# Optimization experiments

Measured on AMD Instinct MI355X. Metric: run time of the kernel, lower is better.

The kernel has to match this reference:

```python
import jax, jax.numpy as jnp
import numpy as np

B, S, H = 1, 2048, 1024
NH, HD = 16, 64          # num heads, head dim (H = NH*HD)
NT = 1024                # param token num (qkv_slot_num = proj_slot_num)


def pattention(x, key_tokens, value_tokens):
    """Pattention with gelu_l2_norm: x:[...,H] -> [...,out]."""
    attn = jnp.einsum('bsh,th->bst', x, key_tokens)          # scale_factor = 1
    g = jax.nn.gelu(attn, approximate=False)                 # torch F.gelu exact
    norm = jnp.linalg.norm(g, axis=-1, keepdims=True)
    w = g / norm * jnp.sqrt(jnp.asarray(g.shape[-1], g.dtype))
    return jnp.einsum('bst,td->bsd', w, value_tokens)


def setup_inputs() -> dict:
    key = jax.random.key(0)
    ks = jax.random.split(key, 9)
    names = ['q_key', 'q_val', 'k_key', 'k_val', 'v_key', 'v_val', 'proj_key', 'proj_val']
    inp = {'x': jax.random.normal(ks[0], (B, S, H), jnp.float32)}
    for i, n in enumerate(names):
        inp[n] = jax.random.normal(ks[i + 1], (NT, H), jnp.float32) * 0.02
    return inp


def reference(x, q_key, q_val, k_key, k_val, v_key, v_val, proj_key, proj_val):
    # Q/K/V via Pattention (token-parameter attention)
    q = pattention(x, q_key, q_val).reshape(B, S, NH, HD)
    k = pattention(x, k_key, k_val).reshape(B, S, NH, HD)
    v = pattention(x, v_key, v_val).reshape(B, S, NH, HD)
    # causal softmax attention, scale = 1/sqrt(head_dim) (flash default)
    scale = 1.0 / jnp.sqrt(jnp.asarray(HD, q.dtype))
    scores = jnp.einsum('bqhd,bkhd->bhqk', q, k) * scale
    causal = jnp.tril(jnp.ones((S, S), dtype=bool))
    scores = jnp.where(causal, scores, jnp.asarray(-1e30, scores.dtype))
    probs = jax.nn.softmax(scores, axis=-1)
    ctx = jnp.einsum('bhqk,bkhd->bqhd', probs, v).reshape(B, S, H)
    # output projection via Pattention
    return pattention(ctx, proj_key, proj_val)
```

## Files before the change

### kernel.cpp

```cpp
#include <hip/hip_runtime.h>
#include <cstdint>
#include <cstddef>

#define S_LEN 2048
#define H_DIM 1024
#define NTOK  1024
#define NHEAD 16
#define HDIM  64
#define NSPLIT 4

typedef __bf16 bf16;
typedef __bf16 bf16x8 __attribute__((ext_vector_type(8)));
typedef __bf16 bf16x4 __attribute__((ext_vector_type(4)));
typedef float  f32x4  __attribute__((ext_vector_type(4)));

#define QSCALE_LOG2E 0.18033688011112042f

static __device__ __forceinline__ f32x4 mfma16(bf16x8 a, bf16x8 b, f32x4 c) {
    return __builtin_amdgcn_mfma_f32_16x16x32_bf16(a, b, c, 0, 0, 0);
}

static __device__ __forceinline__ void async16(const void* gp, void* lp) {
    __builtin_amdgcn_global_load_lds(
        (const __attribute__((address_space(1))) void*)gp,
        (__attribute__((address_space(3))) void*)lp, 16, 0, 0);
}

static __device__ __forceinline__ float fexp2(float x) {
    return __builtin_amdgcn_exp2f(x);
}

struct PrepArgs {
    const float* csrc[6];
    bf16* cdst[6];
    const float* tsrc[4];
    bf16* tdst[4];
    float* ssq;
};
__global__ __launch_bounds__(256) void prep_kernel(PrepArgs a) {
    __shared__ float t[32][33];
    if (blockIdx.y < 6) {
        if (blockIdx.y == 0 && blockIdx.x == 0) {
#pragma unroll
            for (int i = 0; i < 24; ++i) a.ssq[threadIdx.x + i * 256] = 0.0f;
        }
        const float* __restrict__ s = a.csrc[blockIdx.y];
        bf16* __restrict__ d = a.cdst[blockIdx.y];
        size_t i = ((size_t)blockIdx.x * 256 + threadIdx.x) * 4;
        f32x4 v = *(const f32x4*)&s[i];
        bf16x4 o;
        o[0] = (bf16)v[0]; o[1] = (bf16)v[1]; o[2] = (bf16)v[2]; o[3] = (bf16)v[3];
        *(bf16x4*)&d[i] = o;
    } else {
        const int z = blockIdx.y - 6;
        const float* __restrict__ in = a.tsrc[z];
        bf16* __restrict__ out = a.tdst[z];
        const int bx = (blockIdx.x & 31) * 32, by = (blockIdx.x >> 5) * 32;
        const int x = threadIdx.x & 31, y0 = threadIdx.x >> 5;
#pragma unroll
        for (int j = 0; j < 32; j += 8)
            t[y0 + j][x] = in[(size_t)(by + y0 + j) * 1024 + bx + x];
        __syncthreads();
#pragma unroll
        for (int j = 0; j < 32; j += 8)
            out[(size_t)(bx + y0 + j) * 1024 + by + x] = (bf16)t[x][y0 + j];
    }
}

template <int MODE, typename OutT>
struct GemmArgs {
    const bf16* A[3];
    const bf16* B[3];
    OutT* C[3];
    float* S[3];
    bf16* Ct[3];
    float emul[3];
};

template <int MODE, typename OutT>
__global__ __launch_bounds__(256, 3) void gemm_bt(GemmArgs<MODE, OutT> args) {
    constexpr int Kd = 1024, Nd = 1024, BK = 64;
    const bf16* __restrict__ A = args.A[blockIdx.z];
    const bf16* __restrict__ B = args.B[blockIdx.z];
    OutT* __restrict__ C = args.C[blockIdx.z];
    float* __restrict__ S = args.S[blockIdx.z];
    bf16* __restrict__ Ct = args.Ct[blockIdx.z];
    const float emul = args.emul[blockIdx.z];

    __shared__ __align__(16) bf16 As[2][128 * BK];
    __shared__ __align__(16) bf16 Bs[2][64 * BK];

    const int tid = threadIdx.x;
    const int w = tid >> 6, lane = tid & 63, quad = lane >> 4, m16 = lane & 15;
    const int wm = (w >> 1) * 64, wn = (w & 1) * 32;
    const int bm = blockIdx.y * 128, bn = blockIdx.x * 64;

    const int srow = lane >> 3;
    const int sseg = ((lane & 7) ^ srow) * 8;

    auto stage = [&](int buf, int k0) {
        const bf16* Ab = A + (size_t)bm * Kd + k0;
#pragma unroll
        for (int c = 0; c < 4; ++c) {
            int chunk = w * 4 + c;
            async16(Ab + (size_t)(chunk * 8 + srow) * Kd + sseg,
                    &As[buf][chunk * 512]);
        }
        const bf16* Bb = B + (size_t)bn * Kd + k0;
#pragma unroll
        for (int c = 0; c < 2; ++c) {
            int chunk = w * 2 + c;
            async16(Bb + (size_t)(chunk * 8 + srow) * Kd + sseg,
                    &Bs[buf][chunk * 512]);
        }
    };

    f32x4 acc[4][2] = {};
    stage(0, 0);

    for (int k0 = 0; k0 < Kd; k0 += BK) {
        const int buf = (k0 >> 6) & 1;
        asm volatile("s_waitcnt vmcnt(0)" ::: "memory");
        __syncthreads();
        if (k0 + BK < Kd) stage(buf ^ 1, k0 + BK);

        bf16x8 a[2][4], b[2][2];
#pragma unroll
        for (int kc = 0; kc < 2; ++kc) {
#pragma unroll
            for (int i = 0; i < 4; ++i) {
                int row = wm + i * 16 + m16;
                a[kc][i] = *(const bf16x8*)
                    &As[buf][row * 64 + (((kc * 4 + quad) ^ (row & 7)) << 3)];
            }
#pragma unroll
            for (int j = 0; j < 2; ++j) {
                int row = wn + j * 16 + m16;
                b[kc][j] = *(const bf16x8*)
                    &Bs[buf][row * 64 + (((kc * 4 + quad) ^ (row & 7)) << 3)];
            }
        }
#pragma unroll
        for (int kc = 0; kc < 2; ++kc)
#pragma unroll
            for (int i = 0; i < 4; ++i)
#pragma unroll
                for (int j = 0; j < 2; ++j)
                    acc[i][j] = mfma16(a[kc][i], b[kc][j], acc[i][j]);
    }

    if (MODE == 1) {
        float sq[4][4] = {};
#pragma unroll
        for (int i = 0; i < 4; ++i)
#pragma unroll
            for (int j = 0; j < 2; ++j)
#pragma unroll
                for (int r = 0; r < 4; ++r) {
                    int row = bm + wm + i * 16 + quad * 4 + r;
                    int col = bn + wn + j * 16 + m16;
                    float v = acc[i][j][r];
                    v = 0.5f * v * (1.0f + erff(v * 0.70710678118654752f));
                    C[(size_t)row * Nd + col] = (OutT)v;
                    sq[i][r] += v * v;
                }
#pragma unroll
        for (int i = 0; i < 4; ++i)
#pragma unroll
            for (int r = 0; r < 4; ++r) {
                float s2 = sq[i][r];
                s2 += __shfl_xor(s2, 1);
                s2 += __shfl_xor(s2, 2);
                s2 += __shfl_xor(s2, 4);
                s2 += __shfl_xor(s2, 8);
                if (m16 == 0)
                    atomicAdd(&S[bm + wm + i * 16 + quad * 4 + r], s2);
            }
        return;
    }

    float scl[4][4];
#pragma unroll
    for (int i = 0; i < 4; ++i)
#pragma unroll
        for (int r = 0; r < 4; ++r)
            scl[i][r] =
                32.0f * rsqrtf(S[bm + wm + i * 16 + quad * 4 + r]) * emul;

    if (Ct != nullptr) {
#pragma unroll
        for (int i = 0; i < 4; ++i)
#pragma unroll
            for (int j = 0; j < 2; ++j) {
                int k = bm + wm + i * 16 + quad * 4;
                int col = bn + wn + j * 16 + m16;
                bf16x4 o4;
#pragma unroll
                for (int r = 0; r < 4; ++r)
                    o4[r] = (bf16)(acc[i][j][r] * scl[i][r]);
                int kb = k >> 6, c = (k >> 3) & 7, off = k & 7;
                int pos = ((c ^ (col & 7)) << 3) + off;
                *(bf16x4*)&Ct[(size_t)col * 2048 + kb * 64 + pos] = o4;
            }
        return;
    }

#pragma unroll
    for (int i = 0; i < 4; ++i)
#pragma unroll
        for (int j = 0; j < 2; ++j)
#pragma unroll
            for (int r = 0; r < 4; ++r) {
                int row = bm + wm + i * 16 + quad * 4 + r;
                int col = bn + wn + j * 16 + m16;
                C[(size_t)row * Nd + col] = (OutT)(acc[i][j][r] * scl[i][r]);
            }
}

template <int MODE, typename OutT>
__global__ __launch_bounds__(512) void gemm_bt512(GemmArgs<MODE, OutT> args) {
    constexpr int Kd = 1024, Nd = 1024, BK = 64;
    const bf16* __restrict__ A = args.A[blockIdx.z];
    const bf16* __restrict__ B = args.B[blockIdx.z];
    OutT* __restrict__ C = args.C[blockIdx.z];
    float* __restrict__ S = args.S[blockIdx.z];
    const float emul = args.emul[blockIdx.z];

    __shared__ __align__(16) bf16 As[2][128 * BK];
    __shared__ __align__(16) bf16 Bs[2][64 * BK];

    const int tid = threadIdx.x;
    const int w = tid >> 6, lane = tid & 63, quad = lane >> 4, m16 = lane & 15;
    const int wm = (w >> 1) * 32, wn = (w & 1) * 32;
    const int bm = blockIdx.y * 128, bn = blockIdx.x * 64;

    const int srow = lane >> 3;
    const int sseg = ((lane & 7) ^ srow) * 8;

    auto stage = [&](int buf, int k0) {
        const bf16* Ab = A + (size_t)bm * Kd + k0;
#pragma unroll
        for (int c = 0; c < 2; ++c) {
            int chunk = w * 2 + c;
            async16(Ab + (size_t)(chunk * 8 + srow) * Kd + sseg,
                    &As[buf][chunk * 512]);
        }
        const bf16* Bb = B + (size_t)bn * Kd + k0;
        {
            int chunk = w;
            async16(Bb + (size_t)(chunk * 8 + srow) * Kd + sseg,
                    &Bs[buf][chunk * 512]);
        }
    };

    f32x4 acc[2][2] = {};
    stage(0, 0);

    for (int k0 = 0; k0 < Kd; k0 += BK) {
        const int buf = (k0 >> 6) & 1;
        asm volatile("s_waitcnt vmcnt(0)" ::: "memory");
        __syncthreads();
        if (k0 + BK < Kd) stage(buf ^ 1, k0 + BK);

        bf16x8 a[2][2], b[2][2];
#pragma unroll
        for (int kc = 0; kc < 2; ++kc) {
#pragma unroll
            for (int i = 0; i < 2; ++i) {
                int row = wm + i * 16 + m16;
                a[kc][i] = *(const bf16x8*)
                    &As[buf][row * 64 + (((kc * 4 + quad) ^ (row & 7)) << 3)];
            }
#pragma unroll
            for (int j = 0; j < 2; ++j) {
                int row = wn + j * 16 + m16;
                b[kc][j] = *(const bf16x8*)
                    &Bs[buf][row * 64 + (((kc * 4 + quad) ^ (row & 7)) << 3)];
            }
        }
#pragma unroll
        for (int kc = 0; kc < 2; ++kc)
#pragma unroll
            for (int i = 0; i < 2; ++i)
#pragma unroll
                for (int j = 0; j < 2; ++j)
                    acc[i][j] = mfma16(a[kc][i], b[kc][j], acc[i][j]);
    }

    if (MODE == 1) {
        float sq[2][4] = {};
#pragma unroll
        for (int i = 0; i < 2; ++i)
#pragma unroll
            for (int j = 0; j < 2; ++j)
#pragma unroll
                for (int r = 0; r < 4; ++r) {
                    int row = bm + wm + i * 16 + quad * 4 + r;
                    int col = bn + wn + j * 16 + m16;
                    float v = acc[i][j][r];
                    v = 0.5f * v * (1.0f + erff(v * 0.70710678118654752f));
                    C[(size_t)row * Nd + col] = (OutT)v;
                    sq[i][r] += v * v;
                }
#pragma unroll
        for (int i = 0; i < 2; ++i)
#pragma unroll
            for (int r = 0; r < 4; ++r) {
                float s2 = sq[i][r];
                s2 += __shfl_xor(s2, 1);
                s2 += __shfl_xor(s2, 2);
                s2 += __shfl_xor(s2, 4);
                s2 += __shfl_xor(s2, 8);
                if (m16 == 0)
                    atomicAdd(&S[bm + wm + i * 16 + quad * 4 + r], s2);
            }
        return;
    }

    float scl[2][4];
#pragma unroll
    for (int i = 0; i < 2; ++i)
#pragma unroll
        for (int r = 0; r < 4; ++r)
            scl[i][r] =
                32.0f * rsqrtf(S[bm + wm + i * 16 + quad * 4 + r]) * emul;

#pragma unroll
    for (int i = 0; i < 2; ++i)
#pragma unroll
        for (int j = 0; j < 2; ++j)
#pragma unroll
            for (int r = 0; r < 4; ++r) {
                int row = bm + wm + i * 16 + quad * 4 + r;
                int col = bn + wn + j * 16 + m16;
                C[(size_t)row * Nd + col] = (OutT)(acc[i][j][r] * scl[i][r]);
            }
}

struct FlashArgs {
    const bf16* Q;
    const bf16* K;
    const bf16* VtG;
    bf16* op[NSPLIT];
    float* ml;
};

__global__ __launch_bounds__(256, 6) void flash_kernel(FlashArgs fa) {
    const int bid = blockIdx.x;
    const int h = (bid & 7) * 2 + ((bid >> 3) & 1);
    const int s = (bid >> 4) & 3;
    const int qt = 31 - (bid >> 6);
    const int tid = threadIdx.x;
    const int w = tid >> 6, lane = tid & 63, quad = lane >> 4, m16 = lane & 15;
    const int hOff = h * HDIM;

    __shared__ __align__(16) bf16 Pw[4][16][72];

    const bf16* VtH = fa.VtG + (size_t)hOff * 2048;
    bf16* __restrict__ Opart = fa.op[s];

    const int qRow = qt * 64 + w * 16 + m16;
    bf16x8 bq[2];
    bq[0] = *(const bf16x8*)&fa.Q[(size_t)qRow * H_DIM + hOff + quad * 8];
    bq[1] = *(const bf16x8*)&fa.Q[(size_t)qRow * H_DIM + hOff + 32 + quad * 8];

    f32x4 oacc[4] = {};
    float m_i = -1e30f, l_i = 0.0f;

    const int cnt = (qt >= s) ? ((qt - s) >> 2) + 1 : 0;
    for (int i = 0; i < cnt; ++i) {
        const int kt = s + i * 4;
        const int k0 = kt * 64;
        const bool diag = (kt == qt);
        f32x4 sacc[4] = {};
        __builtin_amdgcn_s_setprio(1);
#pragma unroll
        for (int ks = 0; ks < 2; ++ks)
#pragma unroll
            for (int j = 0; j < 4; ++j) {
                bf16x8 ak = *(const bf16x8*)
                    &fa.K[(size_t)(k0 + j * 16 + m16) * H_DIM + hOff +
                          ks * 32 + quad * 8];
                sacc[j] = mfma16(ak, bq[ks], sacc[j]);
            }
        __builtin_amdgcn_s_setprio(0);
        if (diag) {
#pragma unroll
            for (int j = 0; j < 4; ++j)
#pragma unroll
                for (int rr = 0; rr < 4; ++rr) {
                    int kcol = k0 + j * 16 + quad * 4 + rr;
                    if (kcol > qRow) sacc[j][rr] = -1e30f;
                }
        }
        float tj[4];
#pragma unroll
        for (int j = 0; j < 4; ++j)
            tj[j] = fmaxf(fmaxf(sacc[j][0], sacc[j][1]),
                          fmaxf(sacc[j][2], sacc[j][3]));
        float mx = fmaxf(fmaxf(tj[0], tj[1]), fmaxf(tj[2], tj[3]));
        mx = fmaxf(mx, __shfl_xor(mx, 16));
        mx = fmaxf(mx, __shfl_xor(mx, 32));
        if (!__all(mx - m_i <= 11.5f)) {
            float mnew = fmaxf(m_i, mx);
            float alpha = fexp2(m_i - mnew);
            l_i *= alpha;
#pragma unroll
            for (int jd = 0; jd < 4; ++jd)
#pragma unroll
                for (int rr = 0; rr < 4; ++rr) oacc[jd][rr] *= alpha;
            m_i = mnew;
        }
        float lsj[4];
#pragma unroll
        for (int j = 0; j < 4; ++j) {
            bf16x4 pk;
            float p0 = fexp2(sacc[j][0] - m_i);
            float p1 = fexp2(sacc[j][1] - m_i);
            float p2 = fexp2(sacc[j][2] - m_i);
            float p3 = fexp2(sacc[j][3] - m_i);
            pk[0] = (bf16)p0; pk[1] = (bf16)p1;
            pk[2] = (bf16)p2; pk[3] = (bf16)p3;
            lsj[j] = (p0 + p1) + (p2 + p3);
            *(bf16x4*)&Pw[w][m16][j * 16 + quad * 4] = pk;
        }
        float ls = (lsj[0] + lsj[1]) + (lsj[2] + lsj[3]);
        ls += __shfl_xor(ls, 16);
        ls += __shfl_xor(ls, 32);
        l_i += ls;
        __builtin_amdgcn_s_setprio(1);
#pragma unroll
        for (int ks = 0; ks < 2; ++ks) {
            bf16x8 bp = *(const bf16x8*)&Pw[w][m16][ks * 32 + quad * 8];
#pragma unroll
            for (int jd = 0; jd < 4; ++jd) {
                int d = jd * 16 + m16;
                bf16x8 av = *(const bf16x8*)
                    &VtH[(size_t)d * 2048 + k0 +
                         (((ks * 4 + quad) ^ (d & 7)) << 3)];
                oacc[jd] = mfma16(av, bp, oacc[jd]);
            }
        }
        __builtin_amdgcn_s_setprio(0);
    }
#pragma unroll
    for (int jd = 0; jd < 4; ++jd) {
        bf16x4 o4;
#pragma unroll
        for (int rr = 0; rr < 4; ++rr) o4[rr] = (bf16)oacc[jd][rr];
        *(bf16x4*)&Opart[(size_t)qRow * 1024 + hOff + jd * 16 + quad * 4] = o4;
    }
    if (quad == 0) {
        float* p = fa.ml + ((size_t)(s * 2048 + qRow) * 16 + h) * 2;
        p[0] = m_i;
        p[1] = l_i;
    }
}

struct CombArgs {
    const bf16* op[NSPLIT];
    const float* ml;
    bf16* ctx;
    float* ssp;
};
__global__ __launch_bounds__(256) void combine_kernel(CombArgs ca) {
    if (blockIdx.x < 8) ca.ssp[blockIdx.x * 256 + threadIdx.x] = 0.0f;
    const int unit = blockIdx.x * 4 + (threadIdx.x >> 6);
    const int row = unit >> 4, h = unit & 15;
    const int d = threadIdx.x & 63;
    float mv[NSPLIT], lv[NSPLIT], M = -1e30f;
#pragma unroll
    for (int s2 = 0; s2 < NSPLIT; ++s2) {
        const float* p = ca.ml + ((size_t)(s2 * 2048 + row) * 16 + h) * 2;
        mv[s2] = p[0];
        lv[s2] = p[1];
        M = fmaxf(M, mv[s2]);
    }
    float num = 0.0f, den = 0.0f;
#pragma unroll
    for (int s2 = 0; s2 < NSPLIT; ++s2) {
        float e = fexp2(mv[s2] - M);
        den += lv[s2] * e;
        num += e * (float)ca.op[s2][(size_t)row * 1024 + h * 64 + d];
    }
    ca.ctx[(size_t)row * 1024 + h * 64 + d] = (bf16)(num / den);
}

extern "C" void kernel_launch(void* const* d_in, const int* in_sizes, int n_in,
                              void* d_out, int out_size, void* d_ws,
                              size_t ws_size, hipStream_t stream) {
    const float* x = (const float*)d_in[0];
    const float* keysF[4] = {(const float*)d_in[1], (const float*)d_in[3],
                             (const float*)d_in[5], (const float*)d_in[7]};
    const float* valsF[4] = {(const float*)d_in[2], (const float*)d_in[4],
                             (const float*)d_in[6], (const float*)d_in[8]};
    float* out = (float*)d_out;

    char* ws = (char*)d_ws;
    bf16* xb = (bf16*)(ws);
    bf16* g3[3];
    for (int i = 0; i < 3; ++i) g3[i] = (bf16*)(ws + (4ull << 20) + (size_t)i * (4ull << 20));
    bf16* kb16[4], *vT16[4];
    for (int i = 0; i < 4; ++i) {
        kb16[i] = (bf16*)(ws + (16ull << 20) + (size_t)i * (2ull << 20));
        vT16[i] = (bf16*)(ws + (24ull << 20) + (size_t)i * (2ull << 20));
    }
    bf16* qb    = (bf16*)(ws);
    bf16* kbuf  = (bf16*)(ws + (32ull << 20));
    float* mlbuf = (float*)(ws + (20ull << 20));
    bf16* VtG   = (bf16*)(ws + (36ull << 20));
    bf16* ctx   = (bf16*)(ws + (32ull << 20));
    bf16* projg = (bf16*)(ws + (4ull << 20));

    float* SSq = (float*)d_out;
    float* SSp = (float*)(ws + (21ull << 20));

    bf16* opart[NSPLIT];
    for (int i = 0; i < NSPLIT; ++i)
        opart[i] = (bf16*)(ws + (4ull << 20) + (size_t)i * (4ull << 20));

    PrepArgs pa;
    pa.csrc[0] = x;             pa.cdst[0] = xb;
    pa.csrc[1] = x + (1 << 20); pa.cdst[1] = xb + (1 << 20);
    for (int i = 0; i < 4; ++i) { pa.csrc[2 + i] = keysF[i]; pa.cdst[2 + i] = kb16[i]; }
    for (int i = 0; i < 4; ++i) { pa.tsrc[i] = valsF[i]; pa.tdst[i] = vT16[i]; }
    pa.ssq = SSq;
    prep_kernel<<<dim3(1024, 10), 256, 0, stream>>>(pa);

    GemmArgs<1, bf16> g1;
    for (int z = 0; z < 3; ++z) {
        g1.A[z] = xb; g1.B[z] = kb16[z]; g1.C[z] = g3[z];
        g1.S[z] = SSq + z * 2048; g1.Ct[z] = nullptr; g1.emul[z] = 1.0f;
    }
    gemm_bt<1, bf16><<<dim3(16, 16, 3), 256, 0, stream>>>(g1);

    GemmArgs<2, bf16> g2;
    bf16* qkv[3] = {qb, kbuf, qb };
    for (int z = 0; z < 3; ++z) {
        g2.A[z] = g3[z]; g2.B[z] = vT16[z]; g2.C[z] = qkv[z];
        g2.S[z] = SSq + z * 2048;
        g2.Ct[z] = (z == 2) ? VtG : nullptr;
        g2.emul[z] = (z == 0) ? QSCALE_LOG2E : 1.0f;
    }
    gemm_bt<2, bf16><<<dim3(16, 16, 3), 256, 0, stream>>>(g2);

    FlashArgs fla;
    fla.Q = qb; fla.K = kbuf; fla.VtG = VtG; fla.ml = mlbuf;
    for (int i = 0; i < NSPLIT; ++i) fla.op[i] = opart[i];
    flash_kernel<<<dim3(2048), 256, 0, stream>>>(fla);

    CombArgs cba;
    for (int i = 0; i < NSPLIT; ++i) cba.op[i] = opart[i];
    cba.ml = mlbuf; cba.ctx = ctx; cba.ssp = SSp;
    combine_kernel<<<dim3(8192), 256, 0, stream>>>(cba);

    GemmArgs<1, bf16> p1;
    for (int z = 0; z < 3; ++z) {
        p1.A[z] = ctx; p1.B[z] = kb16[3]; p1.C[z] = projg;
        p1.S[z] = SSp; p1.Ct[z] = nullptr; p1.emul[z] = 1.0f;
    }
    gemm_bt512<1, bf16><<<dim3(16, 16, 1), 512, 0, stream>>>(p1);

    GemmArgs<2, float> p2;
    for (int z = 0; z < 3; ++z) {
        p2.A[z] = projg; p2.B[z] = vT16[3]; p2.C[z] = out;
        p2.S[z] = SSp; p2.Ct[z] = nullptr; p2.emul[z] = 1.0f;
    }
    gemm_bt512<2, float><<<dim3(16, 16, 1), 512, 0, stream>>>(p2);
}
```

Baseline: 243.4 us.

## Double-buffer K and V tiles in LDS with async global-to-LDS loads in flash kernel

The flash attention kernel now stages each 64x64 K tile and V^T tile into LDS with async global_load_lds, double-buffered so the next tile is prefetched while the current one is computed. Previously each wave read K and V fragments straight from global memory, and all four waves reloaded the same data. The staging uses an XOR swizzle so LDS reads avoid bank conflicts. In exchange it adds 32KB of LDS and a barrier every iteration, and lowers the launch-bounds occupancy hint from 6 to 3 blocks per SIMD.

Measured after the change: 212.3 us. 12.8% less time.

```diff
diff --git a/kernel.cpp b/kernel.cpp
--- a/kernel.cpp
+++ b/kernel.cpp
@@ -345,7 +345,7 @@
     float* ml;
 };
 
-__global__ __launch_bounds__(256, 6) void flash_kernel(FlashArgs fa) {
+__global__ __launch_bounds__(256, 3) void flash_kernel(FlashArgs fa) {
     const int bid = blockIdx.x;
     const int h = (bid & 7) * 2 + ((bid >> 3) & 1);
     const int s = (bid >> 4) & 3;
@@ -354,10 +354,30 @@
     const int w = tid >> 6, lane = tid & 63, quad = lane >> 4, m16 = lane & 15;
     const int hOff = h * HDIM;
 
+    __shared__ __align__(16) bf16 Ks[2][64 * 64];
+    __shared__ __align__(16) bf16 Vs[2][64 * 64];
     __shared__ __align__(16) bf16 Pw[4][16][72];
 
     const bf16* VtH = fa.VtG + (size_t)hOff * 2048;
     bf16* __restrict__ Opart = fa.op[s];
+
+    const int trow = tid >> 3, tseg8 = (tid & 7) * 8;
+
+    auto stage = [&](int buf, int k0) {
+#pragma unroll
+        for (int c = 0; c < 2; ++c) {
+            int row = c * 32 + trow;
+            int seg = (((tid & 7) ^ (row & 7)) << 3);
+            async16(fa.K + (size_t)(k0 + row) * H_DIM + hOff + seg,
+                    &Ks[buf][row * 64 + tseg8]);
+        }
+#pragma unroll
+        for (int p = 0; p < 2; ++p) {
+            int d = trow + p * 32;
+            async16(VtH + (size_t)d * 2048 + k0 + tseg8,
+                    &Vs[buf][d * 64 + tseg8]);
+        }
+    };
 
     const int qRow = qt * 64 + w * 16 + m16;
     bf16x8 bq[2];
@@ -368,19 +388,26 @@
     float m_i = -1e30f, l_i = 0.0f;
 
     const int cnt = (qt >= s) ? ((qt - s) >> 2) + 1 : 0;
+    if (cnt > 0) {
+        stage(0, s * 64);
+        asm volatile("s_waitcnt vmcnt(0)" ::: "memory");
+        __builtin_amdgcn_s_barrier();
+    }
     for (int i = 0; i < cnt; ++i) {
-        const int kt = s + i * 4;
+        const int kt = s + i * NSPLIT;
         const int k0 = kt * 64;
+        const int cur = i & 1;
         const bool diag = (kt == qt);
+        if (i + 1 < cnt) stage(cur ^ 1, (kt + NSPLIT) * 64);
         f32x4 sacc[4] = {};
         __builtin_amdgcn_s_setprio(1);
 #pragma unroll
         for (int ks = 0; ks < 2; ++ks)
 #pragma unroll
             for (int j = 0; j < 4; ++j) {
+                int row = j * 16 + m16;
                 bf16x8 ak = *(const bf16x8*)
-                    &fa.K[(size_t)(k0 + j * 16 + m16) * H_DIM + hOff +
-                          ks * 32 + quad * 8];
+                    &Ks[cur][row * 64 + (((ks * 4 + quad) ^ (row & 7)) << 3)];
                 sacc[j] = mfma16(ak, bq[ks], sacc[j]);
             }
         __builtin_amdgcn_s_setprio(0);
@@ -436,12 +463,13 @@
             for (int jd = 0; jd < 4; ++jd) {
                 int d = jd * 16 + m16;
                 bf16x8 av = *(const bf16x8*)
-                    &VtH[(size_t)d * 2048 + k0 +
-                         (((ks * 4 + quad) ^ (d & 7)) << 3)];
+                    &Vs[cur][d * 64 + (((ks * 4 + quad) ^ (d & 7)) << 3)];
                 oacc[jd] = mfma16(av, bp, oacc[jd]);
             }
         }
         __builtin_amdgcn_s_setprio(0);
+        asm volatile("s_waitcnt vmcnt(0)" ::: "memory");
+        __builtin_amdgcn_s_barrier();
     }
 #pragma unroll
     for (int jd = 0; jd < 4; ++jd) {
```
